# Performance work log

Measured on AMD Instinct MI355X. Metric: run time of the kernel, lower is better.

## Reference

```python
import jax, jax.numpy as jnp
import numpy as np

N_NODES = 50000
N_EDGES = 800000
D = 128


def setup_inputs() -> dict:
    key = jax.random.key(0)
    ks = jax.random.split(key, 8)
    h = jax.random.normal(ks[0], (N_NODES, D), dtype=jnp.float32)
    src = jax.random.randint(ks[1], (N_EDGES,), 0, N_NODES, dtype=jnp.int64)
    dst = jax.random.randint(ks[2], (N_EDGES,), 0, N_NODES, dtype=jnp.int64)
    # Glorot-ish init for the three GraphConv weights
    scale = 1.0 / np.sqrt(D)
    W0 = jax.random.normal(ks[3], (D, D), dtype=jnp.float32) * scale
    W1 = jax.random.normal(ks[4], (D, D), dtype=jnp.float32) * scale
    W2 = jax.random.normal(ks[5], (D, D), dtype=jnp.float32) * scale
    b0 = jnp.zeros((D,), dtype=jnp.float32)
    b1 = jnp.zeros((D,), dtype=jnp.float32)
    b2 = jnp.zeros((D,), dtype=jnp.float32)
    return {"h": h, "src": src, "dst": dst, "W0": W0, "b0": b0,
            "W1": W1, "b1": b1, "W2": W2, "b2": b2}


def _graph_conv(x, src, dst, W, b, n_nodes):
    """DGL GraphConv, norm='both', activation=ReLU.
    in_feats == out_feats -> aggregate first, then matmul W."""
    ones = jnp.ones_like(src, dtype=x.dtype)
    out_deg = jnp.clip(jax.ops.segment_sum(ones, src, num_segments=n_nodes), 1.0)
    in_deg = jnp.clip(jax.ops.segment_sum(ones, dst, num_segments=n_nodes), 1.0)
    x = x * (out_deg ** -0.5)[:, None]          # src-side normalization
    m = jax.ops.segment_sum(x[src], dst, num_segments=n_nodes)  # sparse aggregation
    m = m * (in_deg ** -0.5)[:, None]           # dst-side normalization
    return jax.nn.relu(m @ W + b)


def reference(h, src, dst, W0, b0, W1, b1, W2, b2):
    n = h.shape[0]
    h = _graph_conv(h, src, dst, W0, b0, n)
    h = _graph_conv(h, src, dst, W1, b1, n)
    h = _graph_conv(h, src, dst, W2, b2, n)
    return h
```

## Files before the change

kernel.cpp:

```cpp
#include <hip/hip_runtime.h>

#define N_NODES 50000
#define N_EDGES 800000
#define D 128
#define CAP 48
#define MS_STRIDE 132

typedef __attribute__((ext_vector_type(4))) float f32x4;
typedef __attribute__((ext_vector_type(8))) short s16x8;

__device__ inline unsigned short f32_to_bf16_rtne(float f) {
    union { float f; unsigned u; } c; c.f = f;
    unsigned u = c.u;
    u += 0x7FFF + ((u >> 16) & 1);
    return (unsigned short)(u >> 16);
}
__device__ inline float bf16_to_f32(unsigned short h) {
    union { unsigned u; float f; } c; c.u = ((unsigned)h) << 16;
    return c.f;
}
__device__ inline unsigned pack_bf2(float a, float b) {
    return (unsigned)f32_to_bf16_rtne(a) | ((unsigned)f32_to_bf16_rtne(b) << 16);
}
__device__ inline void unpack_bf2(unsigned u, float& a, float& b) {
    union { unsigned u; float f; } c0, c1;
    c0.u = u << 16; c1.u = u & 0xFFFF0000u;
    a = c0.f; b = c1.f;
}
__device__ inline void acc_uint4(uint4 v, float* a) {
    float f0, f1;
    unpack_bf2(v.x, f0, f1); a[0] += f0; a[1] += f1;
    unpack_bf2(v.y, f0, f1); a[2] += f0; a[3] += f1;
    unpack_bf2(v.z, f0, f1); a[4] += f0; a[5] += f1;
    unpack_bf2(v.w, f0, f1); a[6] += f0; a[7] += f1;
}


__global__ __launch_bounds__(256) void fill_slots(const int* __restrict__ src,
                                                  const int* __restrict__ dst,
                                                  int* __restrict__ cursor,
                                                  int* __restrict__ cnt_out,
                                                  int* __restrict__ slots) {
    int e = blockIdx.x * 256 + threadIdx.x;
    if (e < N_EDGES) {
        int d = dst[e], s = src[e];
        int p = atomicAdd(&cursor[d], 1);
        if (p < CAP) slots[d * CAP + p] = s;
        atomicAdd(&cnt_out[s], 1);
    }
}


__global__ __launch_bounds__(256) void hconv_norms(const float4* __restrict__ h,
                                                   const int* __restrict__ cursor,
                                                   const int* __restrict__ cnt_out,
                                                   float* __restrict__ s_in,
                                                   float* __restrict__ s_out,
                                                   uint2* __restrict__ hb) {
    int gid = blockIdx.x * 256 + threadIdx.x;
    if (gid >= N_NODES * 32) return;
    int node = gid >> 5;
    float so = rsqrtf(fmaxf((float)cnt_out[node], 1.0f));
    if ((gid & 31) == 0) {
        s_out[node] = so;
        s_in[node]  = rsqrtf(fmaxf((float)cursor[node], 1.0f));
    }
    float4 v = h[gid];
    hb[gid] = make_uint2(pack_bf2(so * v.x, so * v.y), pack_bf2(so * v.z, so * v.w));
}


__global__ __launch_bounds__(256) void pack_w(const float* __restrict__ W0,
                                              const float* __restrict__ W1,
                                              const float* __restrict__ W2,
                                              s16x8* __restrict__ wpk) {
    int tid = threadIdx.x;
    int wid = blockIdx.x * 4 + (tid >> 6);
    if (wid >= 96) return;
    int lane = tid & 63;
    int layer = wid / 32, rem = wid % 32;
    int ct = rem >> 2, ks = rem & 3;
    const float* W = (layer == 0) ? W0 : (layer == 1) ? W1 : W2;
    int col = ct * 16 + (lane & 15);
    int k0  = ks * 32 + (lane >> 4) * 8;
    s16x8 hi, lo;
#pragma unroll
    for (int j = 0; j < 8; j++) {
        float w = W[(k0 + j) * D + col];
        unsigned short h = f32_to_bf16_rtne(w);
        hi[j] = (short)h;
        lo[j] = (short)f32_to_bf16_rtne(w - bf16_to_f32(h));
    }
    int idx = layer * 4096 + (ct * 4 + ks) * 64 + lane;
    wpk[idx]        = hi;
    wpk[idx + 2048] = lo;
}


__global__ __launch_bounds__(256) void fused_layer(const uint4* __restrict__ x,
                                                   const int* __restrict__ slots,
                                                   const int* __restrict__ deg,
                                                   const float* __restrict__ s_in,
                                                   const s16x8* __restrict__ wpk,
                                                   const float* __restrict__ bias,
                                                   const float* __restrict__ s_out,
                                                   float* __restrict__ outf,
                                                   unsigned short* __restrict__ outb) {
    __shared__ float mS[16 * MS_STRIDE];
    int tid = threadIdx.x;
    int row0 = blockIdx.x * 16;

    {
        int nloc = tid >> 4;
        int l    = tid & 15;
        int node = row0 + nloc;
        int dg = min(deg[node], CAP);
        int base = node * CAP;
        int idx0 = (l      < dg) ? slots[base + l]      : 0;
        int idx1 = (16 + l < dg) ? slots[base + 16 + l] : 0;
        int idx2 = (32 + l < dg) ? slots[base + 32 + l] : 0;

        float a[8];
#pragma unroll
        for (int j = 0; j < 8; j++) a[j] = 0.f;

        int e = 0;
        for (; e + 8 <= dg; e += 8) {
            int c = e >> 4, k = e & 15;
            int v = (c == 0) ? idx0 : ((c == 1) ? idx1 : idx2);
            int s0 = __shfl(v, k + 0, 16), s1 = __shfl(v, k + 1, 16);
            int s2 = __shfl(v, k + 2, 16), s3 = __shfl(v, k + 3, 16);
            int s4 = __shfl(v, k + 4, 16), s5 = __shfl(v, k + 5, 16);
            int s6 = __shfl(v, k + 6, 16), s7 = __shfl(v, k + 7, 16);
            uint4 g0 = x[s0 * 16 + l];
            uint4 g1 = x[s1 * 16 + l];
            uint4 g2 = x[s2 * 16 + l];
            uint4 g3 = x[s3 * 16 + l];
            uint4 g4 = x[s4 * 16 + l];
            uint4 g5 = x[s5 * 16 + l];
            uint4 g6 = x[s6 * 16 + l];
            uint4 g7 = x[s7 * 16 + l];
            acc_uint4(g0, a); acc_uint4(g1, a); acc_uint4(g2, a); acc_uint4(g3, a);
            acc_uint4(g4, a); acc_uint4(g5, a); acc_uint4(g6, a); acc_uint4(g7, a);
        }
        for (; e + 4 <= dg; e += 4) {
            int c = e >> 4, k = e & 15;
            int v = (c == 0) ? idx0 : ((c == 1) ? idx1 : idx2);
            int s0 = __shfl(v, k + 0, 16), s1 = __shfl(v, k + 1, 16);
            int s2 = __shfl(v, k + 2, 16), s3 = __shfl(v, k + 3, 16);
            uint4 g0 = x[s0 * 16 + l];
            uint4 g1 = x[s1 * 16 + l];
            uint4 g2 = x[s2 * 16 + l];
            uint4 g3 = x[s3 * 16 + l];
            acc_uint4(g0, a); acc_uint4(g1, a); acc_uint4(g2, a); acc_uint4(g3, a);
        }
        for (; e < dg; e++) {
            int c = e >> 4, k = e & 15;
            int v = (c == 0) ? idx0 : ((c == 1) ? idx1 : idx2);
            int s0 = __shfl(v, k, 16);
            uint4 g0 = x[s0 * 16 + l];
            acc_uint4(g0, a);
        }
        float si = s_in[node];
        float* dp = &mS[nloc * MS_STRIDE + l * 8];
#pragma unroll
        for (int j = 0; j < 8; j++) dp[j] = a[j] * si;
    }
    __syncthreads();

    int wv = tid >> 6;
    int lane = tid & 63;
    int arow = lane & 15, aq = lane >> 4;
    int ct0 = wv * 2, ct1 = ct0 + 1;
    f32x4 acc0 = (f32x4)0.f, acc1 = (f32x4)0.f;

#pragma unroll
    for (int ks = 0; ks < 4; ks++) {
        const float* ap = &mS[arow * MS_STRIDE + ks * 32 + aq * 8];
        s16x8 ahi, alo;
#pragma unroll
        for (int j = 0; j < 8; j++) {
            float av = ap[j];
            unsigned short hh = f32_to_bf16_rtne(av);
            ahi[j] = (short)hh;
            alo[j] = (short)f32_to_bf16_rtne(av - bf16_to_f32(hh));
        }
        int idx0 = (ct0 * 4 + ks) * 64 + lane;
        int idx1 = (ct1 * 4 + ks) * 64 + lane;
        s16x8 b0h = wpk[idx0], b0l = wpk[idx0 + 2048];
        s16x8 b1h = wpk[idx1], b1l = wpk[idx1 + 2048];
        acc0 = __builtin_amdgcn_mfma_f32_16x16x32_bf16(ahi, b0h, acc0, 0, 0, 0);
        acc0 = __builtin_amdgcn_mfma_f32_16x16x32_bf16(alo, b0h, acc0, 0, 0, 0);
        acc0 = __builtin_amdgcn_mfma_f32_16x16x32_bf16(ahi, b0l, acc0, 0, 0, 0);
        acc1 = __builtin_amdgcn_mfma_f32_16x16x32_bf16(ahi, b1h, acc1, 0, 0, 0);
        acc1 = __builtin_amdgcn_mfma_f32_16x16x32_bf16(alo, b1h, acc1, 0, 0, 0);
        acc1 = __builtin_amdgcn_mfma_f32_16x16x32_bf16(ahi, b1l, acc1, 0, 0, 0);
    }

    int crow0 = aq * 4;
    float so4[4];
    if (outb) {
#pragma unroll
        for (int r = 0; r < 4; r++) so4[r] = s_out[row0 + crow0 + r];
    }
    int colA = ct0 * 16 + arow, colB = ct1 * 16 + arow;
    float bA = bias[colA], bB = bias[colB];
#pragma unroll
    for (int r = 0; r < 4; r++) {
        size_t rowoff = (size_t)(row0 + crow0 + r) * D;
        float vA = fmaxf(acc0[r] + bA, 0.f);
        float vB = fmaxf(acc1[r] + bB, 0.f);
        if (outf) { outf[rowoff + colA] = vA; outf[rowoff + colB] = vB; }
        if (outb) {
            outb[rowoff + colA] = f32_to_bf16_rtne(so4[r] * vA);
            outb[rowoff + colB] = f32_to_bf16_rtne(so4[r] * vB);
        }
    }
}


extern "C" void kernel_launch(void* const* d_in, const int* in_sizes, int n_in,
                              void* d_out, int out_size, void* d_ws, size_t ws_size,
                              hipStream_t stream) {
    const float* h  = (const float*)d_in[0];
    const int*  src = (const int*)d_in[1];
    const int*  dst = (const int*)d_in[2];
    const float* W0 = (const float*)d_in[3];
    const float* b0 = (const float*)d_in[4];
    const float* W1 = (const float*)d_in[5];
    const float* b1 = (const float*)d_in[6];
    const float* W2 = (const float*)d_in[7];
    const float* b2 = (const float*)d_in[8];
    float* out = (float*)d_out;

    char* w = (char*)d_ws;
    auto carve = [&](size_t bytes) -> void* {
        void* p = (void*)w;
        w += (bytes + 255) & ~(size_t)255;
        return p;
    };
    int*   cnt     = (int*)carve(2 * N_NODES * sizeof(int));
    int*   cursor  = cnt;
    int*   cnt_out = cnt + N_NODES;
    float* s_in    = (float*)carve(N_NODES * sizeof(float));
    float* s_out   = (float*)carve(N_NODES * sizeof(float));
    int*   slots   = (int*)carve((size_t)N_NODES * CAP * sizeof(int));
    unsigned short* actA = (unsigned short*)carve((size_t)N_NODES * D * 2);
    unsigned short* actB = (unsigned short*)carve((size_t)N_NODES * D * 2);
    s16x8* wpk     = (s16x8*)carve(3 * 4096 * sizeof(s16x8));

    hipMemsetAsync(cnt, 0, 2 * N_NODES * sizeof(int), stream);
    fill_slots<<<(N_EDGES + 255) / 256, 256, 0, stream>>>(src, dst, cursor, cnt_out, slots);
    hconv_norms<<<(N_NODES * 32 + 255) / 256, 256, 0, stream>>>((const float4*)h, cursor, cnt_out,
                                                                s_in, s_out, (uint2*)actA);
    pack_w<<<24, 256, 0, stream>>>(W0, W1, W2, wpk);

    const int GRID = N_NODES / 16;

    fused_layer<<<GRID, 256, 0, stream>>>((const uint4*)actA, slots, cursor, s_in,
                                          wpk, b0, s_out, nullptr, actB);
    fused_layer<<<GRID, 256, 0, stream>>>((const uint4*)actB, slots, cursor, s_in,
                                          wpk + 4096, b1, s_out, nullptr, actA);
    fused_layer<<<GRID, 256, 0, stream>>>((const uint4*)actA, slots, cursor, s_in,
                                          wpk + 8192, b2, s_out, out, nullptr);
}
```

Baseline: 278.2 us.

## Replace out-degree atomics with LDS histograms, merge setup kernels, pad gather tail

Out-degree counting moves from global atomics to per-block shared-memory histograms with 8-bit packed counters. Their partial results are reduced in a kernel that also packs the weights. Setup kernels are merged to cut launches, and s_in is now computed inline from the in-degree. The gather loop pads each neighbor list to a multiple of 8 with a zero sentinel row, which removes the remainder loops at the cost of extra redundant loads. The histogram path writes and reads a ~12.8MB partial buffer and relies on each block's count per node staying under 256.

```diff
diff --git a/kernel.cpp b/kernel.cpp
--- a/kernel.cpp
+++ b/kernel.cpp
@@ -5,6 +5,13 @@
 #define D 128
 #define CAP 48
 #define MS_STRIDE 132
+#define QNODES 12500
+#define QWORDS (QNODES / 4)
+#define HISTB 1024
+#define EPB (N_EDGES / 256)
+#define HWORDS (N_NODES / 4)
+#define FILLB ((N_EDGES + 255) / 256)
+#define REDB ((HWORDS + 255) / 256)
 
 typedef __attribute__((ext_vector_type(4))) float f32x4;
 typedef __attribute__((ext_vector_type(8))) short s16x8;
@@ -36,71 +43,106 @@
 }
 
 
-__global__ __launch_bounds__(256) void fill_slots(const int* __restrict__ src,
-                                                  const int* __restrict__ dst,
-                                                  int* __restrict__ cursor,
-                                                  int* __restrict__ cnt_out,
-                                                  int* __restrict__ slots) {
-    int e = blockIdx.x * 256 + threadIdx.x;
-    if (e < N_EDGES) {
-        int d = dst[e], s = src[e];
-        int p = atomicAdd(&cursor[d], 1);
-        if (p < CAP) slots[d * CAP + p] = s;
-        atomicAdd(&cnt_out[s], 1);
-    }
-}
-
-
-__global__ __launch_bounds__(256) void hconv_norms(const float4* __restrict__ h,
-                                                   const int* __restrict__ cursor,
-                                                   const int* __restrict__ cnt_out,
-                                                   float* __restrict__ s_in,
-                                                   float* __restrict__ s_out,
-                                                   uint2* __restrict__ hb) {
+__global__ __launch_bounds__(256) void build_all(const int* __restrict__ src,
+                                                 const int* __restrict__ dst,
+                                                 int* __restrict__ cursor,
+                                                 unsigned* __restrict__ partial,
+                                                 int* __restrict__ slots) {
+    __shared__ unsigned hist[QWORDS];
+    int b = blockIdx.x;
+    if (b < HISTB) {
+        int q = b >> 8, p = b & 255;
+        int n0 = q * QNODES;
+        for (int i = threadIdx.x; i < QWORDS; i += 256) hist[i] = 0;
+        __syncthreads();
+        int e0 = p * EPB;
+        for (int i = threadIdx.x; i < EPB; i += 256) {
+            int s = src[e0 + i];
+            unsigned r = (unsigned)(s - n0);
+            if (r < (unsigned)QNODES) atomicAdd(&hist[r >> 2], 1u << ((r & 3) * 8));
+        }
+        __syncthreads();
+        unsigned* dstp = partial + (size_t)b * QWORDS;
+        for (int i = threadIdx.x; i < QWORDS; i += 256) dstp[i] = hist[i];
+    } else {
+        int e = (b - HISTB) * 256 + threadIdx.x;
+        if (e < N_EDGES) {
+            int d = dst[e], s = src[e];
+            int pos = atomicAdd(&cursor[d], 1);
+            if (pos < CAP) slots[d * CAP + pos] = s;
+        }
+    }
+}
+
+
+__global__ __launch_bounds__(256) void mid_reduce_pack(const unsigned* __restrict__ partial,
+                                                       float* __restrict__ s_out,
+                                                       const float* __restrict__ W0,
+                                                       const float* __restrict__ W1,
+                                                       const float* __restrict__ W2,
+                                                       s16x8* __restrict__ wpk) {
+    int blk = blockIdx.x;
+    if (blk < REDB) {
+        int w = blk * 256 + threadIdx.x;
+        if (w >= HWORDS) return;
+        int q = w / QWORDS, wq = w - q * QWORDS;
+        const unsigned* base = partial + (size_t)(q * 256) * QWORDS + wq;
+        int c0 = 0, c1 = 0, c2 = 0, c3 = 0;
+        for (int p = 0; p < 256; p++) {
+            unsigned v = base[(size_t)p * QWORDS];
+            c0 += v & 255; c1 += (v >> 8) & 255; c2 += (v >> 16) & 255; c3 += v >> 24;
+        }
+        float4 so;
+        so.x = rsqrtf(fmaxf((float)c0, 1.0f));
+        so.y = rsqrtf(fmaxf((float)c1, 1.0f));
+        so.z = rsqrtf(fmaxf((float)c2, 1.0f));
+        so.w = rsqrtf(fmaxf((float)c3, 1.0f));
+        ((float4*)s_out)[w] = so;
+    } else {
+        int wid = (blk - REDB) * 4 + (threadIdx.x >> 6);
+        if (wid >= 96) return;
+        int lane = threadIdx.x & 63;
+        int layer = wid / 32, rem = wid % 32;
+        int ct = rem >> 2, ks = rem & 3;
+        const float* W = (layer == 0) ? W0 : (layer == 1) ? W1 : W2;
+        int col = ct * 16 + (lane & 15);
+        int k0  = ks * 32 + (lane >> 4) * 8;
+        s16x8 hi, lo;
+#pragma unroll
+        for (int j = 0; j < 8; j++) {
+            float w = W[(k0 + j) * D + col];
+            unsigned short h = f32_to_bf16_rtne(w);
+            hi[j] = (short)h;
+            lo[j] = (short)f32_to_bf16_rtne(w - bf16_to_f32(h));
+        }
+        int idx = layer * 4096 + (ct * 4 + ks) * 64 + lane;
+        wpk[idx]        = hi;
+        wpk[idx + 2048] = lo;
+    }
+}
+
+
+__global__ __launch_bounds__(256) void hconv(const float4* __restrict__ h,
+                                             const float* __restrict__ s_out,
+                                             uint2* __restrict__ hbA,
+                                             uint2* __restrict__ hbB) {
     int gid = blockIdx.x * 256 + threadIdx.x;
-    if (gid >= N_NODES * 32) return;
-    int node = gid >> 5;
-    float so = rsqrtf(fmaxf((float)cnt_out[node], 1.0f));
-    if ((gid & 31) == 0) {
-        s_out[node] = so;
-        s_in[node]  = rsqrtf(fmaxf((float)cursor[node], 1.0f));
-    }
-    float4 v = h[gid];
-    hb[gid] = make_uint2(pack_bf2(so * v.x, so * v.y), pack_bf2(so * v.z, so * v.w));
-}
-
-
-__global__ __launch_bounds__(256) void pack_w(const float* __restrict__ W0,
-                                              const float* __restrict__ W1,
-                                              const float* __restrict__ W2,
-                                              s16x8* __restrict__ wpk) {
-    int tid = threadIdx.x;
-    int wid = blockIdx.x * 4 + (tid >> 6);
-    if (wid >= 96) return;
-    int lane = tid & 63;
-    int layer = wid / 32, rem = wid % 32;
-    int ct = rem >> 2, ks = rem & 3;
-    const float* W = (layer == 0) ? W0 : (layer == 1) ? W1 : W2;
-    int col = ct * 16 + (lane & 15);
-    int k0  = ks * 32 + (lane >> 4) * 8;
-    s16x8 hi, lo;
-#pragma unroll
-    for (int j = 0; j < 8; j++) {
-        float w = W[(k0 + j) * D + col];
-        unsigned short h = f32_to_bf16_rtne(w);
-        hi[j] = (short)h;
-        lo[j] = (short)f32_to_bf16_rtne(w - bf16_to_f32(h));
-    }
-    int idx = layer * 4096 + (ct * 4 + ks) * 64 + lane;
-    wpk[idx]        = hi;
-    wpk[idx + 2048] = lo;
+    const int total = N_NODES * 32;
+    if (gid < total) {
+        float so = s_out[gid >> 5];
+        float4 v = h[gid];
+        hbA[gid] = make_uint2(pack_bf2(so * v.x, so * v.y), pack_bf2(so * v.z, so * v.w));
+    } else if (gid < total + 32) {
+        hbA[total + (gid - total)] = make_uint2(0u, 0u);
+    } else if (gid < total + 64) {
+        hbB[total + (gid - total - 32)] = make_uint2(0u, 0u);
+    }
 }
 
 
 __global__ __launch_bounds__(256) void fused_layer(const uint4* __restrict__ x,
                                                    const int* __restrict__ slots,
                                                    const int* __restrict__ deg,
-                                                   const float* __restrict__ s_in,
                                                    const s16x8* __restrict__ wpk,
                                                    const float* __restrict__ bias,
                                                    const float* __restrict__ s_out,
@@ -114,20 +156,22 @@
         int nloc = tid >> 4;
         int l    = tid & 15;
         int node = row0 + nloc;
-        int dg = min(deg[node], CAP);
+        int dgraw = deg[node];
+        int dg = min(dgraw, CAP);
         int base = node * CAP;
-        int idx0 = (l      < dg) ? slots[base + l]      : 0;
-        int idx1 = (16 + l < dg) ? slots[base + 16 + l] : 0;
-        int idx2 = (32 + l < dg) ? slots[base + 32 + l] : 0;
+        int idx0 = (l      < dg) ? slots[base + l]      : N_NODES;
+        int idx1 = (16 + l < dg) ? slots[base + 16 + l] : N_NODES;
+        int idx2 = (32 + l < dg) ? slots[base + 32 + l] : N_NODES;
 
         float a[8];
 #pragma unroll
         for (int j = 0; j < 8; j++) a[j] = 0.f;
 
-        int e = 0;
-        for (; e + 8 <= dg; e += 8) {
-            int c = e >> 4, k = e & 15;
+        int nr = (dg + 7) >> 3;
+        for (int r = 0; r < nr; r++) {
+            int c = r >> 1;
             int v = (c == 0) ? idx0 : ((c == 1) ? idx1 : idx2);
+            int k = (r & 1) * 8;
             int s0 = __shfl(v, k + 0, 16), s1 = __shfl(v, k + 1, 16);
             int s2 = __shfl(v, k + 2, 16), s3 = __shfl(v, k + 3, 16);
             int s4 = __shfl(v, k + 4, 16), s5 = __shfl(v, k + 5, 16);
@@ -143,25 +187,7 @@
             acc_uint4(g0, a); acc_uint4(g1, a); acc_uint4(g2, a); acc_uint4(g3, a);
             acc_uint4(g4, a); acc_uint4(g5, a); acc_uint4(g6, a); acc_uint4(g7, a);
         }
-        for (; e + 4 <= dg; e += 4) {
-            int c = e >> 4, k = e & 15;
-            int v = (c == 0) ? idx0 : ((c == 1) ? idx1 : idx2);
-            int s0 = __shfl(v, k + 0, 16), s1 = __shfl(v, k + 1, 16);
-            int s2 = __shfl(v, k + 2, 16), s3 = __shfl(v, k + 3, 16);
-            uint4 g0 = x[s0 * 16 + l];
-            uint4 g1 = x[s1 * 16 + l];
-            uint4 g2 = x[s2 * 16 + l];
-            uint4 g3 = x[s3 * 16 + l];
-            acc_uint4(g0, a); acc_uint4(g1, a); acc_uint4(g2, a); acc_uint4(g3, a);
-        }
-        for (; e < dg; e++) {
-            int c = e >> 4, k = e & 15;
-            int v = (c == 0) ? idx0 : ((c == 1) ? idx1 : idx2);
-            int s0 = __shfl(v, k, 16);
-            uint4 g0 = x[s0 * 16 + l];
-            acc_uint4(g0, a);
-        }
-        float si = s_in[node];
+        float si = rsqrtf(fmaxf((float)dgraw, 1.0f));
         float* dp = &mS[nloc * MS_STRIDE + l * 8];
 #pragma unroll
         for (int j = 0; j < 8; j++) dp[j] = a[j] * si;
@@ -239,28 +265,26 @@
         w += (bytes + 255) & ~(size_t)255;
         return p;
     };
-    int*   cnt     = (int*)carve(2 * N_NODES * sizeof(int));
-    int*   cursor  = cnt;
-    int*   cnt_out = cnt + N_NODES;
-    float* s_in    = (float*)carve(N_NODES * sizeof(float));
-    float* s_out   = (float*)carve(N_NODES * sizeof(float));
-    int*   slots   = (int*)carve((size_t)N_NODES * CAP * sizeof(int));
-    unsigned short* actA = (unsigned short*)carve((size_t)N_NODES * D * 2);
-    unsigned short* actB = (unsigned short*)carve((size_t)N_NODES * D * 2);
-    s16x8* wpk     = (s16x8*)carve(3 * 4096 * sizeof(s16x8));
-
-    hipMemsetAsync(cnt, 0, 2 * N_NODES * sizeof(int), stream);
-    fill_slots<<<(N_EDGES + 255) / 256, 256, 0, stream>>>(src, dst, cursor, cnt_out, slots);
-    hconv_norms<<<(N_NODES * 32 + 255) / 256, 256, 0, stream>>>((const float4*)h, cursor, cnt_out,
-                                                                s_in, s_out, (uint2*)actA);
-    pack_w<<<24, 256, 0, stream>>>(W0, W1, W2, wpk);
+    int*      cursor  = (int*)carve(N_NODES * sizeof(int));
+    float*    s_out   = (float*)carve(N_NODES * sizeof(float));
+    int*      slots   = (int*)carve((size_t)N_NODES * CAP * sizeof(int));
+    unsigned* partial = (unsigned*)carve((size_t)HISTB * QWORDS * sizeof(unsigned));
+    unsigned short* actA = (unsigned short*)carve((size_t)(N_NODES + 1) * D * 2);
+    unsigned short* actB = (unsigned short*)carve((size_t)(N_NODES + 1) * D * 2);
+    s16x8*    wpk     = (s16x8*)carve(3 * 4096 * sizeof(s16x8));
+
+    hipMemsetAsync(cursor, 0, N_NODES * sizeof(int), stream);
+    build_all<<<HISTB + FILLB, 256, 0, stream>>>(src, dst, cursor, partial, slots);
+    mid_reduce_pack<<<REDB + 24, 256, 0, stream>>>(partial, s_out, W0, W1, W2, wpk);
+    hconv<<<(N_NODES * 32 + 64 + 255) / 256, 256, 0, stream>>>((const float4*)h, s_out,
+                                                               (uint2*)actA, (uint2*)actB);
 
     const int GRID = N_NODES / 16;
 
-    fused_layer<<<GRID, 256, 0, stream>>>((const uint4*)actA, slots, cursor, s_in,
+    fused_layer<<<GRID, 256, 0, stream>>>((const uint4*)actA, slots, cursor,
                                           wpk, b0, s_out, nullptr, actB);
-    fused_layer<<<GRID, 256, 0, stream>>>((const uint4*)actB, slots, cursor, s_in,
+    fused_layer<<<GRID, 256, 0, stream>>>((const uint4*)actB, slots, cursor,
                                           wpk + 4096, b1, s_out, nullptr, actA);
-    fused_layer<<<GRID, 256, 0, stream>>>((const uint4*)actA, slots, cursor, s_in,
+    fused_layer<<<GRID, 256, 0, stream>>>((const uint4*)actA, slots, cursor,
                                           wpk + 8192, b2, s_out, out, nullptr);
 }
```

Result: faster. 261.0 us (-6.2%).
